# Kernel tuning notes

Hardware: AMD Instinct MI355X
Metric: run time of the kernel (lower is better)

## Reference

```python
import jax, jax.numpy as jnp
import numpy as np

N_HEAD = 16
OUTPUT_DIM = 1024
HEAD_DIM = OUTPUT_DIM // N_HEAD  # 64


def setup_inputs() -> dict:
    key = jax.random.key(0)
    kq, kk, kv = jax.random.split(key, 3)
    B, S, D = 4, 2048, OUTPUT_DIM
    return {
        "Q": jax.random.normal(kq, (B, S, D), dtype=jnp.float32),
        "K": jax.random.normal(kk, (B, S, D), dtype=jnp.float32),
        "V": jax.random.normal(kv, (B, S, D), dtype=jnp.float32),
    }


def reference(Q, K, V):
    # FAITHFUL to the original Keras layer: it reshapes Q into K and V as well
    # (K = reshape(Q, ...), V = reshape(Q, ...)), so the K and V inputs are
    # ignored and attention is computed of Q against itself.
    B, S, _ = Q.shape
    q = Q.reshape(B, S, N_HEAD, HEAD_DIM)  # [B,S,H,D]
    scale = 1.0 / np.sqrt(HEAD_DIM).astype(np.float32)
    # scores: [B,H,S,S]
    scores = jnp.einsum("bshd,bthd->bhst", q, q) * scale
    attn = jax.nn.softmax(scores, axis=-1)
    out = jnp.einsum("bhst,bthd->bshd", attn, q)  # [B,S,H,D]
    # concat of per-head slices along last axis == head-major reshape
    return out.reshape(B, S, N_HEAD * HEAD_DIM)
```

## Files before the change

kernel.cpp:

```cpp
#include <hip/hip_runtime.h>
#include <stdint.h>

#define S_LEN 2048
#define DH    64
#define NH    16
#define DM    1024
#define NBH   64

typedef float    f32x4 __attribute__((ext_vector_type(4)));
typedef _Float16 half8 __attribute__((ext_vector_type(8)));
typedef _Float16 half4 __attribute__((ext_vector_type(4)));

#define GL_LDS_B128(g, l) \
  __builtin_amdgcn_global_load_lds((const __attribute__((address_space(1))) void*)(g), \
                                   (__attribute__((address_space(3))) void*)(l), 16, 0, 0)

__global__ __launch_bounds__(256) void preprocess_kernel(const float* __restrict__ Q,
                                                         _Float16* __restrict__ Qh,
                                                         _Float16* __restrict__ QhT) {
    __shared__ __align__(16) _Float16 tile[64][72];
    const int t  = threadIdx.x;
    const int st = blockIdx.x & 31;
    const int bh = blockIdx.x >> 5;
    const int b = bh >> 4, h = bh & 15;
    const int s0 = st * 64;

    {
        const int r = t >> 2;
        const int c = (t & 3) * 16;
        const float* src = Q + ((size_t)b * S_LEN + s0 + r) * DM + h * DH + c;
        #pragma unroll
        for (int i = 0; i < 4; ++i) {
            const float4 v = ((const float4*)src)[i];
            *(half4*)&tile[r][c + 4 * i] =
                (half4){ (_Float16)v.x, (_Float16)v.y, (_Float16)v.z, (_Float16)v.w };
        }
    }
    __syncthreads();

    {
        const int s = t >> 2;
        const int c = (t & 3) * 16;
        const half8 a = *(const half8*)&tile[s][c];
        const half8 b8 = *(const half8*)&tile[s][c + 8];
        _Float16* dst = Qh + ((size_t)bh * S_LEN + s0 + s) * DH + c;
        *(half8*)dst = a;
        *(half8*)(dst + 8) = b8;
    }

    {
        const int d  = t >> 2;
        const int sg = (t & 3) * 16;
        half8 x0, x1;
        #pragma unroll
        for (int j = 0; j < 8; ++j) {
            x0[j] = tile[sg + j][d];
            x1[j] = tile[sg + 8 + j][d];
        }
        _Float16* dst = QhT + ((size_t)bh * DH + d) * S_LEN + s0 + sg;
        *(half8*)dst = x0;
        *(half8*)(dst + 8) = x1;
    }
}

__global__ __launch_bounds__(256, 4) void attn_v4_kernel(const _Float16* __restrict__ Qh,
                                                         const _Float16* __restrict__ QhT,
                                                         float* __restrict__ out) {
    __shared__ __align__(16) _Float16 KnS[64 * 64];
    __shared__ __align__(16) _Float16 KtS[64 * 64];
    __shared__ __align__(16) _Float16 Pb[4][32 * 64];

    const int tid  = threadIdx.x;
    const int w    = tid >> 6;
    const int lane = tid & 63;
    const int quad = lane >> 4;
    const int l15  = lane & 15;
    const int xq   = l15 & 7;
    const int qblk = blockIdx.x & 15;
    const int bh   = blockIdx.x >> 4;
    const int q0   = qblk * 128 + w * 32;

    const _Float16* qh_bh = Qh + (size_t)bh * S_LEN * DH;
    const _Float16* qt_bh = QhT + (size_t)bh * DH * S_LEN;

    half8 qreg[2][2];
    #pragma unroll
    for (int nch = 0; nch < 2; ++nch) {
        const _Float16* p = qh_bh + (size_t)(q0 + nch * 16 + l15) * DH + quad * 8;
        qreg[nch][0] = *(const half8*)p;
        qreg[nch][1] = *(const half8*)(p + 32);
    }

    const float qs = 0.18033688011112042f;
    float m_c[2];
    #pragma unroll
    for (int nch = 0; nch < 2; ++nch) {
        float part = 0.f;
        #pragma unroll
        for (int s = 0; s < 2; ++s)
            #pragma unroll
            for (int j = 0; j < 8; ++j) { const float x = (float)qreg[nch][s][j]; part += x * x; }
        part += __shfl_xor(part, 16, 64);
        part += __shfl_xor(part, 32, 64);
        m_c[nch] = qs * part;
    }

    const _Float16* kn_src[2]; _Float16* kn_dst[2];
    const _Float16* kt_src[2]; _Float16* kt_dst[2];
    #pragma unroll
    for (int i = 0; i < 2; ++i) {
        const int ch = i * 256 + tid;
        const int row = ch >> 3, c = ch & 7;
        kn_src[i] = qh_bh + row * DH + ((c ^ (row & 7)) * 8);
        kn_dst[i] = &KnS[ch * 8];
        kt_src[i] = qt_bh + (size_t)row * S_LEN + ((c ^ (row & 7)) * 8);
        kt_dst[i] = &KtS[ch * 8];
    }

    f32x4 O[2][4];
    #pragma unroll
    for (int m = 0; m < 2; ++m)
        #pragma unroll
        for (int n = 0; n < 4; ++n) O[m][n] = (f32x4){0.f, 0.f, 0.f, 0.f};
    float lsum[2] = {0.f, 0.f};
    _Float16* Pw = Pb[w];

    for (int t = 0; t < S_LEN / 64; ++t) {
        __syncthreads();
        #pragma unroll
        for (int i = 0; i < 2; ++i) GL_LDS_B128(kn_src[i] + t * (64 * DH), kn_dst[i]);
        #pragma unroll
        for (int i = 0; i < 2; ++i) GL_LDS_B128(kt_src[i] + t * 64, kt_dst[i]);
        __syncthreads();

        #pragma unroll
        for (int mch = 0; mch < 4; ++mch) {
            const half8 a0 = *(const half8*)&KnS[(mch * 16 + l15) * 64 + ((quad ^ xq) * 8)];
            const half8 a1 = *(const half8*)&KnS[(mch * 16 + l15) * 64 + (((4 + quad) ^ xq) * 8)];
            const int wc   = 2 * mch + (quad >> 1);
            const int woff = (quad & 1) * 4;
            #pragma unroll
            for (int nch = 0; nch < 2; ++nch) {
                f32x4 acc = (f32x4){0.f, 0.f, 0.f, 0.f};
                acc = __builtin_amdgcn_mfma_f32_16x16x32_f16(a0, qreg[nch][0], acc, 0, 0, 0);
                acc = __builtin_amdgcn_mfma_f32_16x16x32_f16(a1, qreg[nch][1], acc, 0, 0, 0);
                const float p0 = __builtin_amdgcn_exp2f(__builtin_fmaf(acc[0], qs, -m_c[nch]));
                const float p1 = __builtin_amdgcn_exp2f(__builtin_fmaf(acc[1], qs, -m_c[nch]));
                const float p2 = __builtin_amdgcn_exp2f(__builtin_fmaf(acc[2], qs, -m_c[nch]));
                const float p3 = __builtin_amdgcn_exp2f(__builtin_fmaf(acc[3], qs, -m_c[nch]));
                lsum[nch] += (p0 + p1) + (p2 + p3);
                const half4 hv = (half4){ (_Float16)p0, (_Float16)p1, (_Float16)p2, (_Float16)p3 };
                *(half4*)&Pw[(nch * 16 + l15) * 64 + ((wc ^ xq) * 8) + woff] = hv;
            }
        }

        half8 pf[2][2];
        #pragma unroll
        for (int qb = 0; qb < 2; ++qb) {
            pf[qb][0] = *(const half8*)&Pw[(qb * 16 + l15) * 64 + ((quad ^ xq) * 8)];
            pf[qb][1] = *(const half8*)&Pw[(qb * 16 + l15) * 64 + (((4 + quad) ^ xq) * 8)];
        }
        #pragma unroll
        for (int nch = 0; nch < 4; ++nch) {
            const half8 v0 = *(const half8*)&KtS[(nch * 16 + l15) * 64 + ((quad ^ xq) * 8)];
            const half8 v1 = *(const half8*)&KtS[(nch * 16 + l15) * 64 + (((4 + quad) ^ xq) * 8)];
            #pragma unroll
            for (int qb = 0; qb < 2; ++qb) {
                O[qb][nch] = __builtin_amdgcn_mfma_f32_16x16x32_f16(pf[qb][0], v0, O[qb][nch], 0, 0, 0);
                O[qb][nch] = __builtin_amdgcn_mfma_f32_16x16x32_f16(pf[qb][1], v1, O[qb][nch], 0, 0, 0);
            }
        }
    }

    float lcol[2];
    #pragma unroll
    for (int qb = 0; qb < 2; ++qb) {
        float l = lsum[qb];
        l += __shfl_xor(l, 16, 64);
        l += __shfl_xor(l, 32, 64);
        lcol[qb] = l;
    }
    const int b = bh >> 4, h = bh & 15;
    float* ob = out + (size_t)b * S_LEN * DM + h * DH;
    #pragma unroll
    for (int qb = 0; qb < 2; ++qb) {
        float inv[4];
        #pragma unroll
        for (int r = 0; r < 4; ++r)
            inv[r] = 1.0f / __shfl(lcol[qb], quad * 4 + r, 16);
        #pragma unroll
        for (int nch = 0; nch < 4; ++nch)
            #pragma unroll
            for (int r = 0; r < 4; ++r)
                ob[(size_t)(q0 + qb * 16 + quad * 4 + r) * DM + nch * 16 + l15] = O[qb][nch][r] * inv[r];
    }
}

extern "C" void kernel_launch(void* const* d_in, const int* in_sizes, int n_in,
                              void* d_out, int out_size, void* d_ws, size_t ws_size,
                              hipStream_t stream) {
    const float* Q = (const float*)d_in[0];
    float* out = (float*)d_out;
    _Float16* Qh  = (_Float16*)d_ws;
    _Float16* QhT = Qh + (size_t)NBH * S_LEN * DH;
    preprocess_kernel<<<dim3(NBH * (S_LEN / 64)), dim3(256), 0, stream>>>(Q, Qh, QhT);
    attn_v4_kernel<<<dim3(NBH * (S_LEN / 128)), dim3(256), 0, stream>>>(Qh, QhT, out);
}
```

Baseline: 211.1 us.

## Fuse fp16 conversion and transpose into attention kernel, drop preprocess pass

Removes the separate preprocess kernel that wrote fp16 and transposed copies of Q to workspace. The attention kernel now reads fp32 Q directly each tile, converts it to half in registers, and writes both the row-major and transposed swizzled LDS tiles itself. It also remaps block IDs so that blocks sharing a (batch, head) are spread in a strided order, which is meant to improve L2 locality across XCDs. This saves one launch and the workspace round trip. In exchange, every block re-reads fp32 K/V tiles (twice the bytes of fp16), loses the async global-to-LDS loads, and adds conversion and scattered LDS stores to the inner loop.

```diff
diff --git a/kernel.cpp b/kernel.cpp
--- a/kernel.cpp
+++ b/kernel.cpp
@@ -11,60 +11,7 @@
 typedef _Float16 half8 __attribute__((ext_vector_type(8)));
 typedef _Float16 half4 __attribute__((ext_vector_type(4)));
 
-#define GL_LDS_B128(g, l) \
-  __builtin_amdgcn_global_load_lds((const __attribute__((address_space(1))) void*)(g), \
-                                   (__attribute__((address_space(3))) void*)(l), 16, 0, 0)
-
-__global__ __launch_bounds__(256) void preprocess_kernel(const float* __restrict__ Q,
-                                                         _Float16* __restrict__ Qh,
-                                                         _Float16* __restrict__ QhT) {
-    __shared__ __align__(16) _Float16 tile[64][72];
-    const int t  = threadIdx.x;
-    const int st = blockIdx.x & 31;
-    const int bh = blockIdx.x >> 5;
-    const int b = bh >> 4, h = bh & 15;
-    const int s0 = st * 64;
-
-    {
-        const int r = t >> 2;
-        const int c = (t & 3) * 16;
-        const float* src = Q + ((size_t)b * S_LEN + s0 + r) * DM + h * DH + c;
-        #pragma unroll
-        for (int i = 0; i < 4; ++i) {
-            const float4 v = ((const float4*)src)[i];
-            *(half4*)&tile[r][c + 4 * i] =
-                (half4){ (_Float16)v.x, (_Float16)v.y, (_Float16)v.z, (_Float16)v.w };
-        }
-    }
-    __syncthreads();
-
-    {
-        const int s = t >> 2;
-        const int c = (t & 3) * 16;
-        const half8 a = *(const half8*)&tile[s][c];
-        const half8 b8 = *(const half8*)&tile[s][c + 8];
-        _Float16* dst = Qh + ((size_t)bh * S_LEN + s0 + s) * DH + c;
-        *(half8*)dst = a;
-        *(half8*)(dst + 8) = b8;
-    }
-
-    {
-        const int d  = t >> 2;
-        const int sg = (t & 3) * 16;
-        half8 x0, x1;
-        #pragma unroll
-        for (int j = 0; j < 8; ++j) {
-            x0[j] = tile[sg + j][d];
-            x1[j] = tile[sg + 8 + j][d];
-        }
-        _Float16* dst = QhT + ((size_t)bh * DH + d) * S_LEN + s0 + sg;
-        *(half8*)dst = x0;
-        *(half8*)(dst + 8) = x1;
-    }
-}
-
-__global__ __launch_bounds__(256, 4) void attn_v4_kernel(const _Float16* __restrict__ Qh,
-                                                         const _Float16* __restrict__ QhT,
+__global__ __launch_bounds__(256, 4) void attn_v5_kernel(const float* __restrict__ Q,
                                                          float* __restrict__ out) {
     __shared__ __align__(16) _Float16 KnS[64 * 64];
     __shared__ __align__(16) _Float16 KtS[64 * 64];
@@ -76,19 +23,27 @@
     const int quad = lane >> 4;
     const int l15  = lane & 15;
     const int xq   = l15 & 7;
-    const int qblk = blockIdx.x & 15;
-    const int bh   = blockIdx.x >> 4;
-    const int q0   = qblk * 128 + w * 32;
 
-    const _Float16* qh_bh = Qh + (size_t)bh * S_LEN * DH;
-    const _Float16* qt_bh = QhT + (size_t)bh * DH * S_LEN;
+    const int bid     = blockIdx.x;
+    const int logical = (bid & 7) * 128 + (bid >> 3);
+    const int qblk    = logical & 15;
+    const int bh      = logical >> 4;
+    const int b = bh >> 4, h = bh & 15;
+    const int q0      = qblk * 128 + w * 32;
+
+    const float* qbase = Q + (size_t)b * S_LEN * DM + h * DH;
 
     half8 qreg[2][2];
     #pragma unroll
     for (int nch = 0; nch < 2; ++nch) {
-        const _Float16* p = qh_bh + (size_t)(q0 + nch * 16 + l15) * DH + quad * 8;
-        qreg[nch][0] = *(const half8*)p;
-        qreg[nch][1] = *(const half8*)(p + 32);
+        const float* p = qbase + (size_t)(q0 + nch * 16 + l15) * DM + quad * 8;
+        #pragma unroll
+        for (int s = 0; s < 2; ++s) {
+            const float4 f0 = *(const float4*)(p + s * 32);
+            const float4 f1 = *(const float4*)(p + s * 32 + 4);
+            qreg[nch][s] = (half8){ (_Float16)f0.x, (_Float16)f0.y, (_Float16)f0.z, (_Float16)f0.w,
+                                    (_Float16)f1.x, (_Float16)f1.y, (_Float16)f1.z, (_Float16)f1.w };
+        }
     }
 
     const float qs = 0.18033688011112042f;
@@ -105,16 +60,17 @@
         m_c[nch] = qs * part;
     }
 
-    const _Float16* kn_src[2]; _Float16* kn_dst[2];
-    const _Float16* kt_src[2]; _Float16* kt_dst[2];
+    const int kj0 = (tid & 15) * 4;
+    const int d0  = (tid >> 4) * 4;
+    const float* stage_src = qbase + (size_t)kj0 * DM + d0;
+    _Float16* knp[4];
+    _Float16* ktp[4];
     #pragma unroll
-    for (int i = 0; i < 2; ++i) {
-        const int ch = i * 256 + tid;
-        const int row = ch >> 3, c = ch & 7;
-        kn_src[i] = qh_bh + row * DH + ((c ^ (row & 7)) * 8);
-        kn_dst[i] = &KnS[ch * 8];
-        kt_src[i] = qt_bh + (size_t)row * S_LEN + ((c ^ (row & 7)) * 8);
-        kt_dst[i] = &KtS[ch * 8];
+    for (int i = 0; i < 4; ++i) {
+        const int kr = kj0 + i;
+        knp[i] = &KnS[kr * 64 + (((d0 >> 3) ^ (kr & 7)) * 8) + (d0 & 7)];
+        const int dr = d0 + i;
+        ktp[i] = &KtS[dr * 64 + (((kj0 >> 3) ^ (dr & 7)) * 8) + (kj0 & 7)];
     }
 
     f32x4 O[2][4];
@@ -125,12 +81,26 @@
     float lsum[2] = {0.f, 0.f};
     _Float16* Pw = Pb[w];
 
-    for (int t = 0; t < S_LEN / 64; ++t) {
+    for (int tt = 0; tt < S_LEN / 64; ++tt) {
         __syncthreads();
+
+        float4 rowv[4];
         #pragma unroll
-        for (int i = 0; i < 2; ++i) GL_LDS_B128(kn_src[i] + t * (64 * DH), kn_dst[i]);
+        for (int i = 0; i < 4; ++i)
+            rowv[i] = *(const float4*)(stage_src + (size_t)(tt * 64 + i) * DM);
+        half4 hv[4];
         #pragma unroll
-        for (int i = 0; i < 2; ++i) GL_LDS_B128(kt_src[i] + t * 64, kt_dst[i]);
+        for (int i = 0; i < 4; ++i)
+            hv[i] = (half4){ (_Float16)rowv[i].x, (_Float16)rowv[i].y,
+                             (_Float16)rowv[i].z, (_Float16)rowv[i].w };
+        #pragma unroll
+        for (int i = 0; i < 4; ++i)
+            *(half4*)knp[i] = hv[i];
+        #pragma unroll
+        for (int dd = 0; dd < 4; ++dd) {
+            const half4 tv = (half4){ hv[0][dd], hv[1][dd], hv[2][dd], hv[3][dd] };
+            *(half4*)ktp[dd] = tv;
+        }
         __syncthreads();
 
         #pragma unroll
@@ -149,8 +119,8 @@
                 const float p2 = __builtin_amdgcn_exp2f(__builtin_fmaf(acc[2], qs, -m_c[nch]));
                 const float p3 = __builtin_amdgcn_exp2f(__builtin_fmaf(acc[3], qs, -m_c[nch]));
                 lsum[nch] += (p0 + p1) + (p2 + p3);
-                const half4 hv = (half4){ (_Float16)p0, (_Float16)p1, (_Float16)p2, (_Float16)p3 };
-                *(half4*)&Pw[(nch * 16 + l15) * 64 + ((wc ^ xq) * 8) + woff] = hv;
+                const half4 hvp = (half4){ (_Float16)p0, (_Float16)p1, (_Float16)p2, (_Float16)p3 };
+                *(half4*)&Pw[(nch * 16 + l15) * 64 + ((wc ^ xq) * 8) + woff] = hvp;
             }
         }
 
@@ -180,7 +150,6 @@
         l += __shfl_xor(l, 32, 64);
         lcol[qb] = l;
     }
-    const int b = bh >> 4, h = bh & 15;
     float* ob = out + (size_t)b * S_LEN * DM + h * DH;
     #pragma unroll
     for (int qb = 0; qb < 2; ++qb) {
@@ -201,8 +170,6 @@
                               hipStream_t stream) {
     const float* Q = (const float*)d_in[0];
     float* out = (float*)d_out;
-    _Float16* Qh  = (_Float16*)d_ws;
-    _Float16* QhT = Qh + (size_t)NBH * S_LEN * DH;
-    preprocess_kernel<<<dim3(NBH * (S_LEN / 64)), dim3(256), 0, stream>>>(Q, Qh, QhT);
-    attn_v4_kernel<<<dim3(NBH * (S_LEN / 128)), dim3(256), 0, stream>>>(Qh, QhT, out);
+    (void)d_ws; (void)ws_size;
+    attn_v5_kernel<<<dim3(NBH * (S_LEN / 128)), dim3(256), 0, stream>>>(Q, out);
 }
```

Result: no change. 213.7 us (+1.2%).
